# Performance work log

Measured on AMD Instinct MI355X. Metric: run time of the kernel, lower is better.

Reference implementation:

```python
import jax, jax.numpy as jnp
import numpy as np

NUM_HEADS = 16
HEAD_DIM = 64
HIDDEN = NUM_HEADS * HEAD_DIM


def _rotate_half(x):
    half = x.shape[-1] // 2
    x1, x2 = x[..., :half], x[..., half:]
    return jnp.concatenate([-x2, x1], axis=-1)


def setup_inputs() -> dict:
    key = jax.random.key(0)
    k1, k2, k3, k4, k5 = jax.random.split(key, 5)
    B, T = 2, 2048
    x = jax.random.normal(k1, (B, T, HIDDEN), dtype=jnp.float32)
    # rotary tables (seq_len, head_dim) as in apply_rope docstring
    cos = jax.random.uniform(k2, (T, HEAD_DIM), dtype=jnp.float32)
    sin = jax.random.uniform(k3, (T, HEAD_DIM), dtype=jnp.float32)
    # nn.Linear weights: y = x @ W.T ; scaled for stable fp32 activations
    w_qkv = jax.random.normal(k4, (3 * HIDDEN, HIDDEN), dtype=jnp.float32) * (1.0 / np.sqrt(HIDDEN))
    w_out = jax.random.normal(k5, (HIDDEN, HIDDEN), dtype=jnp.float32) * (1.0 / np.sqrt(HIDDEN))
    return {"x": x, "cos": cos, "sin": sin, "w_qkv": w_qkv, "w_out": w_out}


def reference(x, cos, sin, w_qkv, w_out):
    B, T, C = x.shape
    H, D = NUM_HEADS, HEAD_DIM
    qkv = jnp.einsum("btc,fc->btf", x, w_qkv)          # (B, T, 3C)
    q, k, v = jnp.split(qkv, 3, axis=-1)
    # (B, T, C) -> (B, H, T, D)
    to_heads = lambda t: t.reshape(B, T, H, D).transpose(0, 2, 1, 3)
    q, k, v = to_heads(q), to_heads(k), to_heads(v)
    # RoPE: broadcast cos/sin (T, D) over batch and heads
    cos_b = cos[None, None, :, :]
    sin_b = sin[None, None, :, :]
    q = q * cos_b + _rotate_half(q) * sin_b
    k = k * cos_b + _rotate_half(k) * sin_b
    # causal scaled dot-product attention (dropout_p = 0 in eval)
    scale = 1.0 / np.sqrt(D)
    scores = jnp.einsum("bhqd,bhkd->bhqk", q, k) * scale  # (B, H, T, T)
    causal = jnp.tril(jnp.ones((T, T), dtype=bool))
    scores = jnp.where(causal[None, None], scores, jnp.finfo(scores.dtype).min)
    probs = jax.nn.softmax(scores, axis=-1)
    out = jnp.einsum("bhqk,bhkd->bhqd", probs, v)          # (B, H, T, D)
    out = out.transpose(0, 2, 1, 3).reshape(B, T, C)
    return jnp.einsum("btc,fc->btf", out, w_out)
```

## Files before the change

### kernel.cpp

```cpp
#include <hip/hip_runtime.h>

typedef unsigned short u16;
typedef __bf16 bf16x8 __attribute__((ext_vector_type(8)));
typedef __bf16 bf16x4 __attribute__((ext_vector_type(4)));
typedef float f32x4 __attribute__((ext_vector_type(4)));

__device__ __forceinline__ u16 f2bf(float f) {
    union { float f; unsigned int i; } v; v.f = f;
    unsigned int x = v.i;
    x += 0x7fffu + ((x >> 16) & 1u);
    return (u16)(x >> 16);
}

__device__ __forceinline__ void gl_lds16(const u16* g, u16* l) {
    __builtin_amdgcn_global_load_lds(
        (const __attribute__((address_space(1))) void*)g,
        (__attribute__((address_space(3))) void*)l, 16, 0, 0);
}

__global__ __launch_bounds__(256, 2)
void cvt_xw_kernel(const float* __restrict__ X, const float* __restrict__ Wq,
                   u16* __restrict__ Xb, u16* __restrict__ Wqb)
{
    const int n1 = 4194304 / 4;
    const int n2 = 3145728 / 4;
    int i = blockIdx.x * 256 + threadIdx.x;
    const int stride = gridDim.x * 256;
    for (; i < n1 + n2; i += stride) {
        float4 v;
        ushort4* dst;
        if (i < n1) { v = ((const float4*)X)[i];       dst = (ushort4*)Xb + i; }
        else        { v = ((const float4*)Wq)[i - n1]; dst = (ushort4*)Wqb + (i - n1); }
        ushort4 o;
        o.x = f2bf(v.x); o.y = f2bf(v.y); o.z = f2bf(v.z); o.w = f2bf(v.w);
        *dst = o;
    }
}

__global__ __launch_bounds__(256, 2)
void cvt_w_kernel(const float* __restrict__ W, u16* __restrict__ Wb)
{
    int i = blockIdx.x * 256 + threadIdx.x;
    float4 v = ((const float4*)W)[i];
    ushort4 o;
    o.x = f2bf(v.x); o.y = f2bf(v.y); o.z = f2bf(v.z); o.w = f2bf(v.w);
    ((ushort4*)Wb)[i] = o;
}

__global__ __launch_bounds__(256, 2)
void qkv_rope_kernel(const u16* __restrict__ X, const u16* __restrict__ W,
                     const float* __restrict__ Cos, const float* __restrict__ Sin,
                     u16* __restrict__ Qo, u16* __restrict__ Ko, u16* __restrict__ Vo)
{
    __shared__ __align__(16) u16 As[128 * 64];
    __shared__ __align__(16) u16 Bs[128 * 64];
    const int tid  = threadIdx.x;
    const int lane = tid & 63, wave = tid >> 6;
    const int l15  = lane & 15, q4 = lane >> 4;
    const int wm = (wave >> 1) * 64, wn = (wave & 1) * 64;
    const int m0 = blockIdx.y * 128, n0 = blockIdx.x * 128;
    const int srow = lane >> 3;
    const int scol = ((lane & 7) ^ srow) * 8;

    f32x4 acc[4][4];
    #pragma unroll
    for (int i = 0; i < 4; i++)
        #pragma unroll
        for (int j = 0; j < 4; j++) { f32x4 z = {}; acc[i][j] = z; }

    for (int k0 = 0; k0 < 1024; k0 += 64) {
        __syncthreads();
        #pragma unroll
        for (int i = 0; i < 4; i++) {
            int rb = wave * 32 + i * 8;
            gl_lds16(X + (size_t)(m0 + rb + srow) * 1024 + k0 + scol, As + rb * 64);
            gl_lds16(W + (size_t)(n0 + rb + srow) * 1024 + k0 + scol, Bs + rb * 64);
        }
        __syncthreads();
        #pragma unroll
        for (int ks = 0; ks < 2; ks++) {
            const int ch = (((4 * ks + q4) ^ (l15 & 7)) * 8);
            bf16x8 af[4], bfr[4];
            #pragma unroll
            for (int i = 0; i < 4; i++) {
                af[i]  = *(const bf16x8*)&As[(wm + i * 16 + l15) * 64 + ch];
                bfr[i] = *(const bf16x8*)&Bs[(wn + i * 16 + l15) * 64 + ch];
            }
            #pragma unroll
            for (int mi = 0; mi < 4; mi++)
                #pragma unroll
                for (int ni = 0; ni < 4; ni++)
                    acc[mi][ni] = __builtin_amdgcn_mfma_f32_16x16x32_bf16(
                        af[mi], bfr[ni], acc[mi][ni], 0, 0, 0);
        }
    }

    #pragma unroll
    for (int mi = 0; mi < 4; mi++) {
        #pragma unroll
        for (int r = 0; r < 4; r++) {
            int row = m0 + wm + mi * 16 + q4 * 4 + r;
            int b = row >> 11, t = row & 2047;
            #pragma unroll
            for (int ni = 0; ni < 4; ni++) {
                int col = n0 + wn + ni * 16 + l15;
                float v = acc[mi][ni][r];
                int sec = col >> 10;
                int hh  = (col >> 6) & 15;
                int d   = col & 63;
                if (sec < 2) {
                    float cs = Cos[t * 64 + d];
                    float sn = Sin[t * 64 + d];
                    float partner = acc[mi][ni ^ 2][r];
                    float rot = (d < 32) ? -partner : partner;
                    v = v * cs + rot * sn;
                    u16* dst = (sec == 0) ? Qo : Ko;
                    dst[(((size_t)(b * 16 + hh)) * 2048 + t) * 64 + d] = f2bf(v);
                } else {
                    Vo[(((size_t)(b * 16 + hh)) * 64 + d) * 2048 + t] = f2bf(v);
                }
            }
        }
    }
}

__global__ __launch_bounds__(256, 4)
void attn_kernel(const u16* __restrict__ Q, const u16* __restrict__ Kg,
                 const u16* __restrict__ Vt, u16* __restrict__ Oh)
{
    __shared__ __align__(16) u16 Ks[64 * 64];
    __shared__ __align__(16) u16 Vs[64 * 64];
    __shared__ __align__(16) __bf16 Ps[4][16][72];

    const int bx = blockIdx.x;
    const int qt = 31 - (bx >> 5);
    const int bh = bx & 31;
    const int b = bh >> 4, h = bh & 15;
    const int tid = threadIdx.x, wave = tid >> 6, lane = tid & 63;
    const int l15 = lane & 15, q4 = lane >> 4;
    const int srow = lane >> 3;
    const int scol = ((lane & 7) ^ srow) * 8;

    const size_t head_off = (size_t)bh * 2048 * 64;
    const u16* Qb = Q  + head_off;
    const u16* Kb = Kg + head_off;
    const u16* Vb = Vt + head_off;

    const int qrow0 = qt * 64 + wave * 16;

    bf16x8 qf[2];
    #pragma unroll
    for (int ks = 0; ks < 2; ks++) {
        bf16x8 t = *(const bf16x8*)(Qb + (size_t)(qrow0 + l15) * 64 + ks * 32 + q4 * 8);
        #pragma unroll
        for (int j = 0; j < 8; j++) t[j] = (__bf16)((float)t[j] * 0.125f);
        qf[ks] = t;
    }

    bf16x8 ones;
    #pragma unroll
    for (int j = 0; j < 8; j++) ones[j] = (__bf16)1.0f;

    f32x4 o[4];
    f32x4 ol = {};
    float mstq = -1e30f;
    #pragma unroll
    for (int ni = 0; ni < 4; ni++) { f32x4 z = {}; o[ni] = z; }

    const int nkv = qt + 1;
    for (int it = 0; it < nkv; it++) {
        const int k0 = it * 64;
        __syncthreads();
        #pragma unroll
        for (int i = 0; i < 4; i++) {
            int id = wave * 4 + i;
            if (id < 8)
                gl_lds16(Kb + (size_t)(k0 + id * 8 + srow) * 64 + scol, Ks + id * 8 * 64);
            else
                gl_lds16(Vb + (size_t)((id - 8) * 8 + srow) * 2048 + k0 + scol,
                         Vs + (id - 8) * 8 * 64);
        }
        __syncthreads();

        f32x4 st[4];
        #pragma unroll
        for (int mi = 0; mi < 4; mi++) { f32x4 z = {}; st[mi] = z; }
        #pragma unroll
        for (int ks = 0; ks < 2; ks++) {
            const int ch = (((4 * ks + q4) ^ (l15 & 7)) * 8);
            bf16x8 kf[4];
            #pragma unroll
            for (int mi = 0; mi < 4; mi++)
                kf[mi] = *(const bf16x8*)&Ks[(mi * 16 + l15) * 64 + ch];
            #pragma unroll
            for (int mi = 0; mi < 4; mi++)
                st[mi] = __builtin_amdgcn_mfma_f32_16x16x32_bf16(kf[mi], qf[ks], st[mi], 0, 0, 0);
        }

        float rm = -1e30f;
        if (it == qt) {
            const int tq = qrow0 + l15;
            #pragma unroll
            for (int mi = 0; mi < 4; mi++)
                #pragma unroll
                for (int r = 0; r < 4; r++) {
                    float v = st[mi][r];
                    if (k0 + mi * 16 + q4 * 4 + r > tq) v = -1e30f;
                    st[mi][r] = v;
                    rm = fmaxf(rm, v);
                }
        } else {
            #pragma unroll
            for (int mi = 0; mi < 4; mi++)
                #pragma unroll
                for (int r = 0; r < 4; r++)
                    rm = fmaxf(rm, st[mi][r]);
        }
        rm = fmaxf(rm, __shfl_xor(rm, 16, 64));
        rm = fmaxf(rm, __shfl_xor(rm, 32, 64));

        float mnew  = fmaxf(mstq, rm);
        float alpha = __expf(mstq - mnew);
        mstq = mnew;

        #pragma unroll
        for (int mi = 0; mi < 4; mi++) {
            bf16x4 p4;
            #pragma unroll
            for (int r = 0; r < 4; r++)
                p4[r] = (__bf16)__expf(st[mi][r] - mnew);
            *(bf16x4*)&Ps[wave][l15][mi * 16 + q4 * 4] = p4;
        }

        float ar[4];
        #pragma unroll
        for (int r = 0; r < 4; r++)
            ar[r] = __shfl(alpha, q4 * 4 + r, 64);
        #pragma unroll
        for (int ni = 0; ni < 4; ni++)
            #pragma unroll
            for (int r = 0; r < 4; r++)
                o[ni][r] *= ar[r];
        #pragma unroll
        for (int r = 0; r < 4; r++)
            ol[r] *= ar[r];

        #pragma unroll
        for (int ks = 0; ks < 2; ks++) {
            const int ch = (((4 * ks + q4) ^ (l15 & 7)) * 8);
            bf16x8 pa = *(const bf16x8*)&Ps[wave][l15][ks * 32 + q4 * 8];
            bf16x8 vf[4];
            #pragma unroll
            for (int ni = 0; ni < 4; ni++)
                vf[ni] = *(const bf16x8*)&Vs[(ni * 16 + l15) * 64 + ch];
            #pragma unroll
            for (int ni = 0; ni < 4; ni++)
                o[ni] = __builtin_amdgcn_mfma_f32_16x16x32_bf16(pa, vf[ni], o[ni], 0, 0, 0);
            ol = __builtin_amdgcn_mfma_f32_16x16x32_bf16(pa, ones, ol, 0, 0, 0);
        }
    }

    #pragma unroll
    for (int r = 0; r < 4; r++) {
        int t = qrow0 + q4 * 4 + r;
        float inv = 1.0f / ol[r];
        #pragma unroll
        for (int ni = 0; ni < 4; ni++) {
            int d = ni * 16 + l15;
            Oh[(((size_t)(b * 2048 + t)) * 16 + h) * 64 + d] = f2bf(o[ni][r] * inv);
        }
    }
}

__global__ __launch_bounds__(256, 2)
void outproj_kernel(const u16* __restrict__ A, const u16* __restrict__ W,
                    float* __restrict__ Cout)
{
    __shared__ __align__(16) u16 As[128 * 64];
    __shared__ __align__(16) u16 Bs[64 * 64];
    const int tid  = threadIdx.x;
    const int lane = tid & 63, wave = tid >> 6;
    const int l15  = lane & 15, q4 = lane >> 4;
    const int wm = (wave >> 1) * 64, wn = (wave & 1) * 32;
    const int m0 = blockIdx.y * 128, n0 = blockIdx.x * 64;
    const int srow = lane >> 3;
    const int scol = ((lane & 7) ^ srow) * 8;

    f32x4 acc[4][2];
    #pragma unroll
    for (int i = 0; i < 4; i++)
        #pragma unroll
        for (int j = 0; j < 2; j++) { f32x4 z = {}; acc[i][j] = z; }

    for (int k0 = 0; k0 < 1024; k0 += 64) {
        __syncthreads();
        #pragma unroll
        for (int i = 0; i < 6; i++) {
            int id = wave * 6 + i;
            if (id < 16) {
                int rb = id * 8;
                gl_lds16(A + (size_t)(m0 + rb + srow) * 1024 + k0 + scol, As + rb * 64);
            } else {
                int rb = (id - 16) * 8;
                gl_lds16(W + (size_t)(n0 + rb + srow) * 1024 + k0 + scol, Bs + rb * 64);
            }
        }
        __syncthreads();
        #pragma unroll
        for (int ks = 0; ks < 2; ks++) {
            const int ch = (((4 * ks + q4) ^ (l15 & 7)) * 8);
            bf16x8 af[4], bfr[2];
            #pragma unroll
            for (int i = 0; i < 4; i++)
                af[i] = *(const bf16x8*)&As[(wm + i * 16 + l15) * 64 + ch];
            #pragma unroll
            for (int ni = 0; ni < 2; ni++)
                bfr[ni] = *(const bf16x8*)&Bs[(wn + ni * 16 + l15) * 64 + ch];
            #pragma unroll
            for (int mi = 0; mi < 4; mi++)
                #pragma unroll
                for (int ni = 0; ni < 2; ni++)
                    acc[mi][ni] = __builtin_amdgcn_mfma_f32_16x16x32_bf16(
                        af[mi], bfr[ni], acc[mi][ni], 0, 0, 0);
        }
    }

    #pragma unroll
    for (int mi = 0; mi < 4; mi++)
        #pragma unroll
        for (int r = 0; r < 4; r++) {
            int row = m0 + wm + mi * 16 + q4 * 4 + r;
            #pragma unroll
            for (int ni = 0; ni < 2; ni++) {
                int col = n0 + wn + ni * 16 + l15;
                Cout[(size_t)row * 1024 + col] = acc[mi][ni][r];
            }
        }
}

extern "C" void kernel_launch(void* const* d_in, const int* in_sizes, int n_in,
                              void* d_out, int out_size, void* d_ws, size_t ws_size,
                              hipStream_t stream) {
    (void)in_sizes; (void)n_in; (void)out_size; (void)ws_size;
    const float* x     = (const float*)d_in[0];
    const float* cosp  = (const float*)d_in[1];
    const float* sinp  = (const float*)d_in[2];
    const float* w_qkv = (const float*)d_in[3];
    const float* w_out = (const float*)d_in[4];
    float* out = (float*)d_out;

    const size_t NELEM = (size_t)2 * 2048 * 1024;
    u16* Q   = (u16*)d_out;
    u16* Xb  = (u16*)d_out + NELEM;
    u16* K   = (u16*)d_ws;
    u16* Vt  = K + NELEM;
    u16* Oh  = Vt + NELEM;
    u16* Wqb = Oh;
    u16* Wob = K;

    cvt_xw_kernel<<<7168, 256, 0, stream>>>(x, w_qkv, Xb, Wqb);
    qkv_rope_kernel<<<dim3(24, 32), 256, 0, stream>>>(Xb, Wqb, cosp, sinp, Q, K, Vt);
    attn_kernel<<<1024, 256, 0, stream>>>(Q, K, Vt, Oh);
    cvt_w_kernel<<<1024, 256, 0, stream>>>(w_out, Wob);
    outproj_kernel<<<dim3(16, 32), 256, 0, stream>>>(Oh, Wob, out);
}
```

Baseline: 199.5 us.

## Widen attention KV tile to 128 and remap blocks for XCD locality

The attention kernel now processes 128 keys per iteration instead of 64. This halves the loop trips and the paired __syncthreads barriers, and gives each wave more MFMA work per softmax step; the V tile gets a wider XOR swizzle to match the new layout. Block indices are remapped so that the four heads sharing an XCD-interleaved slot stay together, which is meant to improve K/V reuse in L2. The cost is more LDS and registers per block (launch bounds drop from 4 to 3 blocks per CU), plus wasted masked work on the diagonal tile when the query tile is even.

```diff
diff --git a/kernel.cpp b/kernel.cpp
--- a/kernel.cpp
+++ b/kernel.cpp
@@ -124,22 +124,24 @@
     }
 }
 
-__global__ __launch_bounds__(256, 4)
+__global__ __launch_bounds__(256, 3)
 void attn_kernel(const u16* __restrict__ Q, const u16* __restrict__ Kg,
                  const u16* __restrict__ Vt, u16* __restrict__ Oh)
 {
-    __shared__ __align__(16) u16 Ks[64 * 64];
-    __shared__ __align__(16) u16 Vs[64 * 64];
-    __shared__ __align__(16) __bf16 Ps[4][16][72];
+    __shared__ __align__(16) u16 Ks[128 * 64];
+    __shared__ __align__(16) u16 Vs[64 * 128];
+    __shared__ __align__(16) __bf16 Ps[4][16][136];
 
     const int bx = blockIdx.x;
-    const int qt = 31 - (bx >> 5);
-    const int bh = bx & 31;
+    const int xcd = bx & 7;
+    const int i8  = bx >> 3;
+    const int bh  = xcd * 4 + (i8 & 3);
+    const int qt  = 31 - (i8 >> 2);
     const int b = bh >> 4, h = bh & 15;
     const int tid = threadIdx.x, wave = tid >> 6, lane = tid & 63;
     const int l15 = lane & 15, q4 = lane >> 4;
     const int srow = lane >> 3;
-    const int scol = ((lane & 7) ^ srow) * 8;
+    const int sKcol = ((lane & 7) ^ srow) * 8;
 
     const size_t head_off = (size_t)bh * 2048 * 64;
     const u16* Qb = Q  + head_off;
@@ -167,54 +169,68 @@
     #pragma unroll
     for (int ni = 0; ni < 4; ni++) { f32x4 z = {}; o[ni] = z; }
 
-    const int nkv = qt + 1;
+    const int nkv = (qt >> 1) + 1;
     for (int it = 0; it < nkv; it++) {
-        const int k0 = it * 64;
-        __syncthreads();
-        #pragma unroll
-        for (int i = 0; i < 4; i++) {
-            int id = wave * 4 + i;
-            if (id < 8)
-                gl_lds16(Kb + (size_t)(k0 + id * 8 + srow) * 64 + scol, Ks + id * 8 * 64);
-            else
-                gl_lds16(Vb + (size_t)((id - 8) * 8 + srow) * 2048 + k0 + scol,
-                         Vs + (id - 8) * 8 * 64);
-        }
-        __syncthreads();
-
-        f32x4 st[4];
-        #pragma unroll
-        for (int mi = 0; mi < 4; mi++) { f32x4 z = {}; st[mi] = z; }
+        const int k0 = it * 128;
+        __syncthreads();
+        #pragma unroll
+        for (int i = 0; i < 8; i++) {
+            int id = wave * 8 + i;
+            if (id < 16) {
+                int rb = id * 8;
+                gl_lds16(Kb + (size_t)(k0 + rb + srow) * 64 + sKcol, Ks + rb * 64);
+            } else {
+                int rb = (id - 16) * 4;
+                int d  = rb + (lane >> 4);
+                int cl = ((lane & 15) ^ (d & 15)) * 8;
+                gl_lds16(Vb + (size_t)d * 2048 + k0 + cl, Vs + rb * 128);
+            }
+        }
+        __syncthreads();
+
+        f32x4 st[2][4];
+        #pragma unroll
+        for (int hf = 0; hf < 2; hf++)
+            #pragma unroll
+            for (int mi = 0; mi < 4; mi++) { f32x4 z = {}; st[hf][mi] = z; }
         #pragma unroll
         for (int ks = 0; ks < 2; ks++) {
             const int ch = (((4 * ks + q4) ^ (l15 & 7)) * 8);
-            bf16x8 kf[4];
-            #pragma unroll
-            for (int mi = 0; mi < 4; mi++)
-                kf[mi] = *(const bf16x8*)&Ks[(mi * 16 + l15) * 64 + ch];
-            #pragma unroll
-            for (int mi = 0; mi < 4; mi++)
-                st[mi] = __builtin_amdgcn_mfma_f32_16x16x32_bf16(kf[mi], qf[ks], st[mi], 0, 0, 0);
+            #pragma unroll
+            for (int hf = 0; hf < 2; hf++) {
+                bf16x8 kf[4];
+                #pragma unroll
+                for (int mi = 0; mi < 4; mi++)
+                    kf[mi] = *(const bf16x8*)&Ks[(hf * 64 + mi * 16 + l15) * 64 + ch];
+                #pragma unroll
+                for (int mi = 0; mi < 4; mi++)
+                    st[hf][mi] = __builtin_amdgcn_mfma_f32_16x16x32_bf16(
+                        kf[mi], qf[ks], st[hf][mi], 0, 0, 0);
+            }
         }
 
         float rm = -1e30f;
-        if (it == qt) {
+        if (it == nkv - 1) {
             const int tq = qrow0 + l15;
             #pragma unroll
-            for (int mi = 0; mi < 4; mi++)
-                #pragma unroll
-                for (int r = 0; r < 4; r++) {
-                    float v = st[mi][r];
-                    if (k0 + mi * 16 + q4 * 4 + r > tq) v = -1e30f;
-                    st[mi][r] = v;
-                    rm = fmaxf(rm, v);
-                }
+            for (int hf = 0; hf < 2; hf++)
+                #pragma unroll
+                for (int mi = 0; mi < 4; mi++)
+                    #pragma unroll
+                    for (int r = 0; r < 4; r++) {
+                        float v = st[hf][mi][r];
+                        if (k0 + hf * 64 + mi * 16 + q4 * 4 + r > tq) v = -1e30f;
+                        st[hf][mi][r] = v;
+                        rm = fmaxf(rm, v);
+                    }
         } else {
             #pragma unroll
-            for (int mi = 0; mi < 4; mi++)
-                #pragma unroll
-                for (int r = 0; r < 4; r++)
-                    rm = fmaxf(rm, st[mi][r]);
+            for (int hf = 0; hf < 2; hf++)
+                #pragma unroll
+                for (int mi = 0; mi < 4; mi++)
+                    #pragma unroll
+                    for (int r = 0; r < 4; r++)
+                        rm = fmaxf(rm, st[hf][mi][r]);
         }
         rm = fmaxf(rm, __shfl_xor(rm, 16, 64));
         rm = fmaxf(rm, __shfl_xor(rm, 32, 64));
@@ -224,13 +240,15 @@
         mstq = mnew;
 
         #pragma unroll
-        for (int mi = 0; mi < 4; mi++) {
-            bf16x4 p4;
-            #pragma unroll
-            for (int r = 0; r < 4; r++)
-                p4[r] = (__bf16)__expf(st[mi][r] - mnew);
-            *(bf16x4*)&Ps[wave][l15][mi * 16 + q4 * 4] = p4;
-        }
+        for (int hf = 0; hf < 2; hf++)
+            #pragma unroll
+            for (int mi = 0; mi < 4; mi++) {
+                bf16x4 p4;
+                #pragma unroll
+                for (int r = 0; r < 4; r++)
+                    p4[r] = (__bf16)__expf(st[hf][mi][r] - mnew);
+                *(bf16x4*)&Ps[wave][l15][hf * 64 + mi * 16 + q4 * 4] = p4;
+            }
 
         float ar[4];
         #pragma unroll
@@ -246,13 +264,14 @@
             ol[r] *= ar[r];
 
         #pragma unroll
-        for (int ks = 0; ks < 2; ks++) {
-            const int ch = (((4 * ks + q4) ^ (l15 & 7)) * 8);
+        for (int ks = 0; ks < 4; ks++) {
             bf16x8 pa = *(const bf16x8*)&Ps[wave][l15][ks * 32 + q4 * 8];
             bf16x8 vf[4];
             #pragma unroll
-            for (int ni = 0; ni < 4; ni++)
-                vf[ni] = *(const bf16x8*)&Vs[(ni * 16 + l15) * 64 + ch];
+            for (int ni = 0; ni < 4; ni++) {
+                const int pc = (((ks * 4 + q4) ^ l15) * 8);
+                vf[ni] = *(const bf16x8*)&Vs[(ni * 16 + l15) * 128 + pc];
+            }
             #pragma unroll
             for (int ni = 0; ni < 4; ni++)
                 o[ni] = __builtin_amdgcn_mfma_f32_16x16x32_bf16(pa, vf[ni], o[ni], 0, 0, 0);
```

New measurement: 190.4 us. -4.6%, faster.
